# Kernel optimization log

Measured on AMD Instinct MI355X. Metric: run time of the kernel, lower is better.

## Reference

```python
import jax, jax.numpy as jnp
import numpy as np

V = 0.1


def _swap_np():
    d = 2
    s = np.zeros((d * d, d * d))
    for i in range(d):
        for j in range(d):
            s[i * d + j, j * d + i] = 1.0
    k, I = np.kron, np.eye
    s0123 = k(I(d ** 2), s)
    s01234 = k(s0123, I(d))
    s0123456 = k(s01234, s)
    s01234567 = k(s0123456, I(d))
    s0123456789 = k(s01234567, s)
    s012345678911 = k(s0123456789, I(d ** 2))
    s01 = k(s, I(d ** 10))
    s12 = k(k(I(d), s), I(d ** 9))
    s23 = k(k(I(d ** 2), s), I(d ** 8))
    s34 = k(k(I(d ** 3), s), I(d ** 7))
    s45 = k(k(I(d ** 4), s), I(d ** 6))
    s56 = k(k(I(d ** 5), s), I(d ** 5))
    s67 = k(k(I(d ** 6), s), I(d ** 4))
    s78 = k(k(I(d ** 7), s), I(d ** 3))
    s89 = k(k(I(d ** 8), s), I(d ** 2))
    s90 = k(k(I(d ** 9), s), I(d))
    s11 = k(I(d ** 10), s)
    chain = [s01, s12, s23, s34, s45, s56, s67, s78, s89, s90, s11,
             s90, s89, s78, s67, s56, s45, s34, s23, s12, s01]
    swap_far = chain[0]
    for mat in chain[1:]:
        swap_far = swap_far @ mat
    return swap_far @ s012345678911


def _obj_np():
    p = np.zeros((4, 4, 4, 4))
    for q in range(4):
        for w in range(4):
            for e in range(4):
                for r in range(4):
                    if q != w and w != e and e != r and q != r:
                        if q == e or w == r:
                            if q == e and w == r:
                                p[q, w, e, r] = (1 - V) / 2 ** 8
                            else:
                                p[q, w, e, r] = (3 + 5 * V) / (2 ** 8 * 3)
                        else:
                            p[q, w, e, r] = (3 + 13 * V) / (2 ** 8 * 3)
                    else:
                        p[q, w, e, r] = (1 - V) / 2 ** 8
    return p


SWAP = jnp.asarray(_swap_np(), dtype=jnp.float32)   # [4096, 4096] permutation
OBJ = jnp.asarray(_obj_np(), dtype=jnp.float32)     # [4, 4, 4, 4] target distribution
TRIU_R, TRIU_C = np.triu_indices(8, k=1)            # 28 strictly-upper entries, row-major


def setup_inputs() -> dict:
    key = jax.random.key(0)
    # small init keeps POVM element M4 = I - M1 - M2 - M3 near-PSD so the KL log is finite
    params = 0.1 * jax.random.normal(key, (121,), dtype=jnp.float32)
    return {"params": params}


def _generate_state(a):
    a = jnp.exp(a)
    a = a / jnp.linalg.norm(a)                       # F.normalize(dim=0)
    psi = jnp.concatenate([a[0:1], jnp.zeros(3, a.dtype), a[1:5]])  # [8]
    # 4-fold tensor product -> [4096]
    return jnp.kron(jnp.kron(jnp.kron(psi, psi), psi), psi)


def _generate_povm(x):
    eigen = jax.nn.softmax(x[:32].reshape(4, 8), axis=0)  # eigenvalues sum to 1 per column
    offd = x[32:116].reshape(3, 28)

    def make(e, od):
        A = jnp.zeros((8, 8), x.dtype).at[TRIU_R, TRIU_C].set(od)
        A = A - A.T                                  # antisymmetric generator
        U = jax.scipy.linalg.expm(A)                 # orthogonal
        return (U * e[None, :]) @ U.T                # U diag(e) U^T

    m012 = jax.vmap(make)(eigen[:3], offd)           # [3, 8, 8]
    m3 = jnp.eye(8, dtype=x.dtype) - m012.sum(axis=0)
    return jnp.concatenate([m012, m3[None]], axis=0)  # [4, 8, 8]


def reference(params):
    state = _generate_state(params[0:5])             # [4096]
    state = SWAP @ state
    rou = jnp.outer(state, state)                    # [4096, 4096] density matrix
    m = _generate_povm(params[5:121])                # [4, 8, 8]
    # trace(rou @ (Mq (x) Mw (x) Me (x) Mr)) via per-leg contraction instead of
    # 256 dense 4096x4096 matmuls: rou[I,J] * Ma[J,I] with I=(i,j,k,l), J=(m,n,o,p)
    R = rou.reshape((8,) * 8)
    result = jnp.einsum('ijklmnop,qmi,wnj,eok,rpl->qwer', R, m, m, m, m)  # [4,4,4,4]
    y = jnp.sum(OBJ * jnp.log(OBJ / result))         # KL divergence
    return y, result, m
```

## Files before the change

### kernel.cpp

```cpp
#include <hip/hip_runtime.h>
#include <math.h>

#define NT 256


__global__ __launch_bounds__(NT) void qu4_all(const float* __restrict__ P,
                                              float* __restrict__ out)
{
    const int tid  = threadIdx.x;
    const int wave = tid >> 6;
    const int lane = tid & 63;

    __shared__ __align__(16) float XTs[3][96];
    __shared__ __align__(16) float Urow[3][96];
    __shared__ __align__(16) float Esh[32];
    __shared__ __align__(16) float psiF[8];
    __shared__ __align__(16) float Mf[256];
    __shared__ __align__(16) float Tc2[3072];
    __shared__ __align__(16) float Gs[21056];
    __shared__ __align__(16) float Hs[5184];
    __shared__ __align__(16) float HTs[5184];
    __shared__ float redC[16];

    if (wave < 3) {
        const int r = lane >> 3, c = lane & 7;
        float Brow[8];
        #pragma unroll
        for (int u = 0; u < 8; u++) {
            if (u == r)     Brow[u] = 0.f;
            else if (r < u) Brow[u] =  P[37 + wave*28 + (7*r - (r*(r-1))/2 + u - r - 1)];
            else            Brow[u] = -P[37 + wave*28 + (7*u - (u*(u-1))/2 + r - u - 1)];
        }
        float x = ((r == c) ? 1.f : 0.f) + Brow[c] * (1.f / 12.f);
        #pragma unroll
        for (int k = 11; k >= 1; --k) {
            XTs[wave][c*12 + r] = x;
            float4 a0 = *(const float4*)&XTs[wave][c*12];
            float4 a1 = *(const float4*)&XTs[wave][c*12 + 4];
            float d = Brow[0]*a0.x + Brow[1]*a0.y + Brow[2]*a0.z + Brow[3]*a0.w
                    + Brow[4]*a1.x + Brow[5]*a1.y + Brow[6]*a1.z + Brow[7]*a1.w;
            x = ((r == c) ? 1.f : 0.f) + d * (1.f / (float)k);
        }
        Urow[wave][r*12 + c] = x;
    } else {
        if (lane < 8) {
            float x0 = P[5 + lane], x1 = P[13 + lane], x2 = P[21 + lane], x3 = P[29 + lane];
            float mx = fmaxf(fmaxf(x0, x1), fmaxf(x2, x3));
            float e0 = expf(x0-mx), e1 = expf(x1-mx), e2 = expf(x2-mx), e3 = expf(x3-mx);
            float s = e0 + e1 + e2 + e3;
            Esh[lane] = e0/s; Esh[8+lane] = e1/s; Esh[16+lane] = e2/s; Esh[24+lane] = e3/s;
        } else if (lane == 8) {
            float av[5]; float ss = 0.f;
            #pragma unroll
            for (int i = 0; i < 5; i++) { av[i] = expf(P[i]); ss += av[i]*av[i]; }
            float inv = 1.f / sqrtf(ss);
            psiF[0] = av[0]*inv; psiF[1] = 0.f; psiF[2] = 0.f; psiF[3] = 0.f;
            psiF[4] = av[1]*inv; psiF[5] = av[2]*inv; psiF[6] = av[3]*inv; psiF[7] = av[4]*inv;
        }
    }
    __syncthreads();

    {
        const int a = wave, r = lane >> 3, c = lane & 7;
        float m;
        if (a < 3) {
            float4 r0 = *(const float4*)&Urow[a][r*12], r1 = *(const float4*)&Urow[a][r*12+4];
            float4 c0 = *(const float4*)&Urow[a][c*12], c1 = *(const float4*)&Urow[a][c*12+4];
            float4 e0 = *(const float4*)&Esh[a*8],      e1 = *(const float4*)&Esh[a*8+4];
            m = r0.x*e0.x*c0.x + r0.y*e0.y*c0.y + r0.z*e0.z*c0.z + r0.w*e0.w*c0.w
              + r1.x*e1.x*c1.x + r1.y*e1.y*c1.y + r1.z*e1.z*c1.z + r1.w*e1.w*c1.w;
        } else {
            float s = 0.f;
            #pragma unroll
            for (int a2 = 0; a2 < 3; a2++) {
                float4 r0 = *(const float4*)&Urow[a2][r*12], r1 = *(const float4*)&Urow[a2][r*12+4];
                float4 c0 = *(const float4*)&Urow[a2][c*12], c1 = *(const float4*)&Urow[a2][c*12+4];
                float4 e0 = *(const float4*)&Esh[a2*8],      e1 = *(const float4*)&Esh[a2*8+4];
                s += r0.x*e0.x*c0.x + r0.y*e0.y*c0.y + r0.z*e0.z*c0.z + r0.w*e0.w*c0.w
                   + r1.x*e1.x*c1.x + r1.y*e1.y*c1.y + r1.z*e1.z*c1.z + r1.w*e1.w*c1.w;
            }
            m = ((r == c) ? 1.f : 0.f) - s;
        }
        Mf[a*64 + lane] = m;
        out[257 + a*64 + lane] = m;
    }
    __syncthreads();

    {
        const int a = tid >> 6, m = (tid >> 3) & 7, j = tid & 7;
        const int j0 = j >> 2, j1 = (j >> 1) & 1;
        float4 m0 = *(const float4*)&Mf[a*64 + m*8], m1 = *(const float4*)&Mf[a*64 + m*8 + 4];
        float mav[8] = {m0.x,m0.y,m0.z,m0.w, m1.x,m1.y,m1.z,m1.w};
        float4 q0 = *(const float4*)&psiF[0], q1 = *(const float4*)&psiF[4];
        float ps[8] = {q0.x,q0.y,q0.z,q0.w, q1.x,q1.y,q1.z,q1.w};
        float pA[4], pB[4];
        #pragma unroll
        for (int c1 = 0; c1 < 2; c1++)
            #pragma unroll
            for (int i1 = 0; i1 < 2; i1++)
                pA[c1*2+i1] = j0 ? ps[c1*4+i1*2+1] : ps[c1*4+i1*2];
        #pragma unroll
        for (int i2 = 0; i2 < 2; i2++)
            #pragma unroll
            for (int c2 = 0; c2 < 2; c2++)
                pB[i2*2+c2] = j1 ? ps[i2*4+2+c2] : ps[i2*4+c2];
        #pragma unroll
        for (int h = 0; h < 8; h++) {
            const int c1 = h >> 2, c2 = (h >> 1) & 1, r4 = h & 1;
            float v = 0.f;
            #pragma unroll
            for (int i1 = 0; i1 < 2; i1++)
                #pragma unroll
                for (int i2 = 0; i2 < 2; i2++)
                    v += mav[r4*4 + i1*2 + i2] * pA[c1*2+i1] * pB[i2*2+c2];
            Tc2[h*384 + a*96 + m*12 + j] = v;
        }
    }
    __syncthreads();

    if (tid < 128) {
        const int p = tid >> 3, m = tid & 7;
        const int a = p >> 2, b = p & 3;
        float Tv[8][8];
        #pragma unroll
        for (int h = 0; h < 8; h++) {
            float4 t0 = *(const float4*)&Tc2[h*384 + a*96 + m*12];
            float4 t1 = *(const float4*)&Tc2[h*384 + a*96 + m*12 + 4];
            Tv[h][0]=t0.x; Tv[h][1]=t0.y; Tv[h][2]=t0.z; Tv[h][3]=t0.w;
            Tv[h][4]=t1.x; Tv[h][5]=t1.y; Tv[h][6]=t1.z; Tv[h][7]=t1.w;
        }
        float mb[64];
        #pragma unroll
        for (int q = 0; q < 16; q++) {
            float4 v = *(const float4*)&Mf[b*64 + q*4];
            mb[q*4]=v.x; mb[q*4+1]=v.y; mb[q*4+2]=v.z; mb[q*4+3]=v.w;
        }
        #pragma unroll
        for (int n = 0; n < 8; n++) {
            float acc[16];
            #pragma unroll
            for (int t = 0; t < 16; t++) {
                const int h  = (t>>3)*4 + ((t>>2)&1)*2 + (t&1);
                const int r3 = (t>>1)&1;
                acc[t] = mb[n*8 + r3]     * Tv[h][r3]
                       + mb[n*8 + 2 + r3] * Tv[h][2 + r3]
                       + mb[n*8 + 4 + r3] * Tv[h][4 + r3]
                       + mb[n*8 + 6 + r3] * Tv[h][6 + r3];
            }
            float* gp = &Gs[p*1316 + m*164 + n*20];
            *(float4*)&gp[0]  = make_float4(acc[0],  acc[1],  acc[2],  acc[3]);
            *(float4*)&gp[4]  = make_float4(acc[4],  acc[5],  acc[6],  acc[7]);
            *(float4*)&gp[8]  = make_float4(acc[8],  acc[9],  acc[10], acc[11]);
            *(float4*)&gp[12] = make_float4(acc[12], acc[13], acc[14], acc[15]);
        }
    }
    __syncthreads();

    if (tid < 128) {
        const int p = tid >> 3, g = tid & 7;
        const int c1 = g >> 2, c2 = (g >> 1) & 1, r3 = g & 1;
        float4 q0 = *(const float4*)&psiF[0], q1 = *(const float4*)&psiF[4];
        float ps[8] = {q0.x,q0.y,q0.z,q0.w, q1.x,q1.y,q1.z,q1.w};
        float pr[4];
        #pragma unroll
        for (int xx = 0; xx < 4; xx++) pr[xx] = r3 ? ps[4+xx] : ps[xx];
        float acc[2][16];
        #pragma unroll
        for (int t = 0; t < 16; t++) { acc[0][t] = 0.f; acc[1][t] = 0.f; }
        #pragma unroll
        for (int m1 = 0; m1 < 2; m1++)
        #pragma unroll
        for (int m2 = 0; m2 < 2; m2++)
        #pragma unroll
        for (int n0 = 0; n0 < 2; n0++)
        #pragma unroll
        for (int n1 = 0; n1 < 2; n1++) {
            const int m = c2*4 + m1*2 + m2;
            const int n = n0*4 + n1*2 + c1;
            const float* gp = &Gs[p*1316 + m*164 + n*20];
            float4 g0 = *(const float4*)&gp[0],  g1 = *(const float4*)&gp[4];
            float4 g2 = *(const float4*)&gp[8],  g3 = *(const float4*)&gp[12];
            const float w1 = pr[m1*2 + n0];
            const float wa = w1 * ps[m2*4 + n1*2];
            const float wb = w1 * ps[m2*4 + n1*2 + 1];
            float gv[16] = {g0.x,g0.y,g0.z,g0.w, g1.x,g1.y,g1.z,g1.w,
                            g2.x,g2.y,g2.z,g2.w, g3.x,g3.y,g3.z,g3.w};
            #pragma unroll
            for (int t = 0; t < 16; t++) { acc[0][t] += wa*gv[t]; acc[1][t] += wb*gv[t]; }
        }
        #pragma unroll
        for (int r4 = 0; r4 < 2; r4++) {
            const int tV = c1*8 + c2*4 + r3*2 + r4;
            float* hb = &Hs[p*324 + tV*20];
            *(float4*)&hb[0]  = make_float4(acc[r4][0],  acc[r4][1],  acc[r4][2],  acc[r4][3]);
            *(float4*)&hb[4]  = make_float4(acc[r4][4],  acc[r4][5],  acc[r4][6],  acc[r4][7]);
            *(float4*)&hb[8]  = make_float4(acc[r4][8],  acc[r4][9],  acc[r4][10], acc[r4][11]);
            *(float4*)&hb[12] = make_float4(acc[r4][12], acc[r4][13], acc[r4][14], acc[r4][15]);
            #pragma unroll
            for (int t = 0; t < 16; t++) HTs[p*324 + t*20 + tV] = acc[r4][t];
        }
    }
    __syncthreads();

    {
        const int tile = tid >> 4, tv = tid & 15;
        const int tp = tile >> 2, tq = tile & 3;
        float4 hp[4][4];
        #pragma unroll
        for (int i = 0; i < 4; i++) {
            const float* hb = &Hs[(tp*4 + i)*324 + tv*20];
            hp[i][0] = *(const float4*)&hb[0];  hp[i][1] = *(const float4*)&hb[4];
            hp[i][2] = *(const float4*)&hb[8];  hp[i][3] = *(const float4*)&hb[12];
        }
        float acc[4][4];
        #pragma unroll
        for (int jq = 0; jq < 4; jq++) {
            const float* tb = &HTs[(tq*4 + jq)*324 + tv*20];
            float4 h0 = *(const float4*)&tb[0],  h1 = *(const float4*)&tb[4];
            float4 h2 = *(const float4*)&tb[8],  h3 = *(const float4*)&tb[12];
            #pragma unroll
            for (int i = 0; i < 4; i++) {
                acc[i][jq] = hp[i][0].x*h0.x + hp[i][0].y*h0.y + hp[i][0].z*h0.z + hp[i][0].w*h0.w
                           + hp[i][1].x*h1.x + hp[i][1].y*h1.y + hp[i][1].z*h1.z + hp[i][1].w*h1.w
                           + hp[i][2].x*h2.x + hp[i][2].y*h2.y + hp[i][2].z*h2.z + hp[i][2].w*h2.w
                           + hp[i][3].x*h3.x + hp[i][3].y*h3.y + hp[i][3].z*h3.z + hp[i][3].w*h3.w;
            }
        }
        #pragma unroll
        for (int i = 0; i < 4; i++)
            #pragma unroll
            for (int j = 0; j < 4; j++) {
                float v = acc[i][j];
                v += __shfl_xor(v, 1, 64);
                v += __shfl_xor(v, 2, 64);
                v += __shfl_xor(v, 4, 64);
                v += __shfl_xor(v, 8, 64);
                acc[i][j] = v;
            }
        if (tv == 0) {
            float kl = 0.f;
            #pragma unroll
            for (int i = 0; i < 4; i++)
                #pragma unroll
                for (int j = 0; j < 4; j++) {
                    const int idx = (tp*4 + i)*16 + (tq*4 + j);
                    const float Cv = acc[i][j];
                    out[1 + idx] = Cv;
                    const int q = (idx>>6)&3, w = (idx>>4)&3, e = (idx>>2)&3, rr = idx&3;
                    const float OA = 0.9f/256.f, OB = 3.5f/768.f, OC = 4.3f/768.f;
                    float obj;
                    if (q != w && w != e && e != rr && q != rr)
                        obj = (q == e || w == rr) ? ((q == e && w == rr) ? OA : OB) : OC;
                    else obj = OA;
                    kl += obj * logf(obj / Cv);
                }
            redC[tile] = kl;
        }
    }
    __syncthreads();
    if (tid == 0) {
        float s = 0.f;
        #pragma unroll
        for (int i = 0; i < 16; i++) s += redC[i];
        out[0] = s;
    }
}

extern "C" void kernel_launch(void* const* d_in, const int* in_sizes, int n_in,
                              void* d_out, int out_size, void* d_ws, size_t ws_size,
                              hipStream_t stream)
{
    const float* P = (const float*)d_in[0];
    float* out = (float*)d_out;
    qu4_all<<<1, NT, 0, stream>>>(P, out);
}
```

Before: 16.05 us.

## Shorten expm Taylor series, register-only columns, drop barrier, spread stages over 256 threads

The matrix exponential now runs one thread per column. Each thread keeps its own 8x8 generator and column in registers, cutting the Taylor series from 12 terms to 10 and removing the LDS round-trips through XTs. One __syncthreads is removed because each wave computes and consumes its own Mf slice. The G and H contraction stages are split across all 256 threads instead of 128, and the KL log/objective work is spread across 16 lanes with a shuffle reduction. The shorter Taylor series may reduce accuracy for larger generator norms, and the removed barrier depends on each wave reading only the Mf rows it wrote itself.

```diff
diff --git a/kernel.cpp b/kernel.cpp
--- a/kernel.cpp
+++ b/kernel.cpp
@@ -11,8 +11,7 @@
     const int wave = tid >> 6;
     const int lane = tid & 63;
 
-    __shared__ __align__(16) float XTs[3][96];
-    __shared__ __align__(16) float Urow[3][96];
+    __shared__ __align__(16) float Ucol[240];
     __shared__ __align__(16) float Esh[32];
     __shared__ __align__(16) float psiF[8];
     __shared__ __align__(16) float Mf[256];
@@ -22,27 +21,41 @@
     __shared__ __align__(16) float HTs[5184];
     __shared__ float redC[16];
 
-    if (wave < 3) {
-        const int r = lane >> 3, c = lane & 7;
-        float Brow[8];
-        #pragma unroll
-        for (int u = 0; u < 8; u++) {
-            if (u == r)     Brow[u] = 0.f;
-            else if (r < u) Brow[u] =  P[37 + wave*28 + (7*r - (r*(r-1))/2 + u - r - 1)];
-            else            Brow[u] = -P[37 + wave*28 + (7*u - (u*(u-1))/2 + r - u - 1)];
-        }
-        float x = ((r == c) ? 1.f : 0.f) + Brow[c] * (1.f / 12.f);
-        #pragma unroll
-        for (int k = 11; k >= 1; --k) {
-            XTs[wave][c*12 + r] = x;
-            float4 a0 = *(const float4*)&XTs[wave][c*12];
-            float4 a1 = *(const float4*)&XTs[wave][c*12 + 4];
-            float d = Brow[0]*a0.x + Brow[1]*a0.y + Brow[2]*a0.z + Brow[3]*a0.w
-                    + Brow[4]*a1.x + Brow[5]*a1.y + Brow[6]*a1.z + Brow[7]*a1.w;
-            x = ((r == c) ? 1.f : 0.f) + d * (1.f / (float)k);
-        }
-        Urow[wave][r*12 + c] = x;
-    } else {
+    if (wave == 0 && lane < 24) {
+        const int a = lane >> 3, c = lane & 7;
+        const float* Pb = P + 37 + a * 28;
+        float B[8][8];
+        #pragma unroll
+        for (int r = 0; r < 8; r++) {
+            B[r][r] = 0.f;
+            #pragma unroll
+            for (int u = r + 1; u < 8; u++) {
+                float v = Pb[7*r - (r*(r-1))/2 + u - r - 1];
+                B[r][u] = v;  B[u][r] = -v;
+            }
+        }
+        float e[8], col[8];
+        #pragma unroll
+        for (int u = 0; u < 8; u++) { e[u] = (u == c) ? 1.f : 0.f; col[u] = e[u]; }
+        #pragma unroll
+        for (int k = 9; k >= 1; --k) {
+            float nc[8];
+            #pragma unroll
+            for (int r = 0; r < 8; r++) {
+                float s0 = B[r][0]*col[0] + B[r][1]*col[1];
+                float s1 = B[r][2]*col[2] + B[r][3]*col[3];
+                float s2 = B[r][4]*col[4] + B[r][5]*col[5];
+                float s3 = B[r][6]*col[6] + B[r][7]*col[7];
+                nc[r] = (s0 + s1) + (s2 + s3);
+            }
+            const float ik = 1.f / (float)k;
+            #pragma unroll
+            for (int r = 0; r < 8; r++) col[r] = e[r] + nc[r] * ik;
+        }
+        float* uc = &Ucol[a*80 + c*8];
+        *(float4*)&uc[0] = make_float4(col[0], col[1], col[2], col[3]);
+        *(float4*)&uc[4] = make_float4(col[4], col[5], col[6], col[7]);
+    } else if (wave == 1) {
         if (lane < 8) {
             float x0 = P[5 + lane], x1 = P[13 + lane], x2 = P[21 + lane], x3 = P[29 + lane];
             float mx = fmaxf(fmaxf(x0, x1), fmaxf(x2, x3));
@@ -64,30 +77,31 @@
         const int a = wave, r = lane >> 3, c = lane & 7;
         float m;
         if (a < 3) {
-            float4 r0 = *(const float4*)&Urow[a][r*12], r1 = *(const float4*)&Urow[a][r*12+4];
-            float4 c0 = *(const float4*)&Urow[a][c*12], c1 = *(const float4*)&Urow[a][c*12+4];
-            float4 e0 = *(const float4*)&Esh[a*8],      e1 = *(const float4*)&Esh[a*8+4];
-            m = r0.x*e0.x*c0.x + r0.y*e0.y*c0.y + r0.z*e0.z*c0.z + r0.w*e0.w*c0.w
-              + r1.x*e1.x*c1.x + r1.y*e1.y*c1.y + r1.z*e1.z*c1.z + r1.w*e1.w*c1.w;
+            float4 e0 = *(const float4*)&Esh[a*8], e1 = *(const float4*)&Esh[a*8+4];
+            float ev[8] = {e0.x,e0.y,e0.z,e0.w, e1.x,e1.y,e1.z,e1.w};
+            float s = 0.f;
+            #pragma unroll
+            for (int u = 0; u < 8; u++)
+                s += Ucol[a*80 + u*8 + r] * ev[u] * Ucol[a*80 + u*8 + c];
+            m = s;
         } else {
             float s = 0.f;
             #pragma unroll
             for (int a2 = 0; a2 < 3; a2++) {
-                float4 r0 = *(const float4*)&Urow[a2][r*12], r1 = *(const float4*)&Urow[a2][r*12+4];
-                float4 c0 = *(const float4*)&Urow[a2][c*12], c1 = *(const float4*)&Urow[a2][c*12+4];
-                float4 e0 = *(const float4*)&Esh[a2*8],      e1 = *(const float4*)&Esh[a2*8+4];
-                s += r0.x*e0.x*c0.x + r0.y*e0.y*c0.y + r0.z*e0.z*c0.z + r0.w*e0.w*c0.w
-                   + r1.x*e1.x*c1.x + r1.y*e1.y*c1.y + r1.z*e1.z*c1.z + r1.w*e1.w*c1.w;
+                float4 e0 = *(const float4*)&Esh[a2*8], e1 = *(const float4*)&Esh[a2*8+4];
+                float ev[8] = {e0.x,e0.y,e0.z,e0.w, e1.x,e1.y,e1.z,e1.w};
+                #pragma unroll
+                for (int u = 0; u < 8; u++)
+                    s += Ucol[a2*80 + u*8 + r] * ev[u] * Ucol[a2*80 + u*8 + c];
             }
             m = ((r == c) ? 1.f : 0.f) - s;
         }
         Mf[a*64 + lane] = m;
         out[257 + a*64 + lane] = m;
     }
-    __syncthreads();
-
-    {
-        const int a = tid >> 6, m = (tid >> 3) & 7, j = tid & 7;
+
+    {
+        const int a = wave, m = lane >> 3, j = lane & 7;
         const int j0 = j >> 2, j1 = (j >> 1) & 1;
         float4 m0 = *(const float4*)&Mf[a*64 + m*8], m1 = *(const float4*)&Mf[a*64 + m*8 + 4];
         float mav[8] = {m0.x,m0.y,m0.z,m0.w, m1.x,m1.y,m1.z,m1.w};
@@ -118,8 +132,8 @@
     }
     __syncthreads();
 
-    if (tid < 128) {
-        const int p = tid >> 3, m = tid & 7;
+    {
+        const int p = tid >> 4, m = (tid >> 1) & 7, nh = tid & 1;
         const int a = p >> 2, b = p & 3;
         float Tv[8][8];
         #pragma unroll
@@ -129,23 +143,26 @@
             Tv[h][0]=t0.x; Tv[h][1]=t0.y; Tv[h][2]=t0.z; Tv[h][3]=t0.w;
             Tv[h][4]=t1.x; Tv[h][5]=t1.y; Tv[h][6]=t1.z; Tv[h][7]=t1.w;
         }
-        float mb[64];
-        #pragma unroll
-        for (int q = 0; q < 16; q++) {
-            float4 v = *(const float4*)&Mf[b*64 + q*4];
-            mb[q*4]=v.x; mb[q*4+1]=v.y; mb[q*4+2]=v.z; mb[q*4+3]=v.w;
-        }
-        #pragma unroll
-        for (int n = 0; n < 8; n++) {
+        float mb[4][8];
+        #pragma unroll
+        for (int n4 = 0; n4 < 4; n4++) {
+            float4 v0 = *(const float4*)&Mf[b*64 + (nh*4 + n4)*8];
+            float4 v1 = *(const float4*)&Mf[b*64 + (nh*4 + n4)*8 + 4];
+            mb[n4][0]=v0.x; mb[n4][1]=v0.y; mb[n4][2]=v0.z; mb[n4][3]=v0.w;
+            mb[n4][4]=v1.x; mb[n4][5]=v1.y; mb[n4][6]=v1.z; mb[n4][7]=v1.w;
+        }
+        #pragma unroll
+        for (int n4 = 0; n4 < 4; n4++) {
+            const int n = nh*4 + n4;
             float acc[16];
             #pragma unroll
             for (int t = 0; t < 16; t++) {
                 const int h  = (t>>3)*4 + ((t>>2)&1)*2 + (t&1);
                 const int r3 = (t>>1)&1;
-                acc[t] = mb[n*8 + r3]     * Tv[h][r3]
-                       + mb[n*8 + 2 + r3] * Tv[h][2 + r3]
-                       + mb[n*8 + 4 + r3] * Tv[h][4 + r3]
-                       + mb[n*8 + 6 + r3] * Tv[h][6 + r3];
+                acc[t] = mb[n4][r3]   * Tv[h][r3]
+                       + mb[n4][2+r3] * Tv[h][2+r3]
+                       + mb[n4][4+r3] * Tv[h][4+r3]
+                       + mb[n4][6+r3] * Tv[h][6+r3];
             }
             float* gp = &Gs[p*1316 + m*164 + n*20];
             *(float4*)&gp[0]  = make_float4(acc[0],  acc[1],  acc[2],  acc[3]);
@@ -156,17 +173,17 @@
     }
     __syncthreads();
 
-    if (tid < 128) {
-        const int p = tid >> 3, g = tid & 7;
+    {
+        const int p = tid >> 4, g = (tid >> 1) & 7, hh = tid & 1;
         const int c1 = g >> 2, c2 = (g >> 1) & 1, r3 = g & 1;
         float4 q0 = *(const float4*)&psiF[0], q1 = *(const float4*)&psiF[4];
         float ps[8] = {q0.x,q0.y,q0.z,q0.w, q1.x,q1.y,q1.z,q1.w};
         float pr[4];
         #pragma unroll
         for (int xx = 0; xx < 4; xx++) pr[xx] = r3 ? ps[4+xx] : ps[xx];
-        float acc[2][16];
-        #pragma unroll
-        for (int t = 0; t < 16; t++) { acc[0][t] = 0.f; acc[1][t] = 0.f; }
+        float acc0[8], acc1[8];
+        #pragma unroll
+        for (int t = 0; t < 8; t++) { acc0[t] = 0.f; acc1[t] = 0.f; }
         #pragma unroll
         for (int m1 = 0; m1 < 2; m1++)
         #pragma unroll
@@ -177,27 +194,28 @@
         for (int n1 = 0; n1 < 2; n1++) {
             const int m = c2*4 + m1*2 + m2;
             const int n = n0*4 + n1*2 + c1;
-            const float* gp = &Gs[p*1316 + m*164 + n*20];
-            float4 g0 = *(const float4*)&gp[0],  g1 = *(const float4*)&gp[4];
-            float4 g2 = *(const float4*)&gp[8],  g3 = *(const float4*)&gp[12];
+            const float* gp = &Gs[p*1316 + m*164 + n*20 + hh*8];
+            float4 g0 = *(const float4*)&gp[0], g1 = *(const float4*)&gp[4];
             const float w1 = pr[m1*2 + n0];
             const float wa = w1 * ps[m2*4 + n1*2];
             const float wb = w1 * ps[m2*4 + n1*2 + 1];
-            float gv[16] = {g0.x,g0.y,g0.z,g0.w, g1.x,g1.y,g1.z,g1.w,
-                            g2.x,g2.y,g2.z,g2.w, g3.x,g3.y,g3.z,g3.w};
-            #pragma unroll
-            for (int t = 0; t < 16; t++) { acc[0][t] += wa*gv[t]; acc[1][t] += wb*gv[t]; }
-        }
-        #pragma unroll
-        for (int r4 = 0; r4 < 2; r4++) {
-            const int tV = c1*8 + c2*4 + r3*2 + r4;
-            float* hb = &Hs[p*324 + tV*20];
-            *(float4*)&hb[0]  = make_float4(acc[r4][0],  acc[r4][1],  acc[r4][2],  acc[r4][3]);
-            *(float4*)&hb[4]  = make_float4(acc[r4][4],  acc[r4][5],  acc[r4][6],  acc[r4][7]);
-            *(float4*)&hb[8]  = make_float4(acc[r4][8],  acc[r4][9],  acc[r4][10], acc[r4][11]);
-            *(float4*)&hb[12] = make_float4(acc[r4][12], acc[r4][13], acc[r4][14], acc[r4][15]);
-            #pragma unroll
-            for (int t = 0; t < 16; t++) HTs[p*324 + t*20 + tV] = acc[r4][t];
+            float gv[8] = {g0.x,g0.y,g0.z,g0.w, g1.x,g1.y,g1.z,g1.w};
+            #pragma unroll
+            for (int t = 0; t < 8; t++) { acc0[t] += wa*gv[t]; acc1[t] += wb*gv[t]; }
+        }
+        {
+            const int tV0 = c1*8 + c2*4 + r3*2;
+            float* hb0 = &Hs[p*324 + tV0*20 + hh*8];
+            *(float4*)&hb0[0] = make_float4(acc0[0], acc0[1], acc0[2], acc0[3]);
+            *(float4*)&hb0[4] = make_float4(acc0[4], acc0[5], acc0[6], acc0[7]);
+            float* hb1 = &Hs[p*324 + (tV0+1)*20 + hh*8];
+            *(float4*)&hb1[0] = make_float4(acc1[0], acc1[1], acc1[2], acc1[3]);
+            *(float4*)&hb1[4] = make_float4(acc1[4], acc1[5], acc1[6], acc1[7]);
+            #pragma unroll
+            for (int t = 0; t < 8; t++) {
+                HTs[p*324 + (hh*8 + t)*20 + tV0]     = acc0[t];
+                HTs[p*324 + (hh*8 + t)*20 + tV0 + 1] = acc1[t];
+            }
         }
     }
     __syncthreads();
@@ -237,25 +255,27 @@
                 v += __shfl_xor(v, 8, 64);
                 acc[i][j] = v;
             }
-        if (tv == 0) {
-            float kl = 0.f;
-            #pragma unroll
-            for (int i = 0; i < 4; i++)
-                #pragma unroll
-                for (int j = 0; j < 4; j++) {
-                    const int idx = (tp*4 + i)*16 + (tq*4 + j);
-                    const float Cv = acc[i][j];
-                    out[1 + idx] = Cv;
-                    const int q = (idx>>6)&3, w = (idx>>4)&3, e = (idx>>2)&3, rr = idx&3;
-                    const float OA = 0.9f/256.f, OB = 3.5f/768.f, OC = 4.3f/768.f;
-                    float obj;
-                    if (q != w && w != e && e != rr && q != rr)
-                        obj = (q == e || w == rr) ? ((q == e && w == rr) ? OA : OB) : OC;
-                    else obj = OA;
-                    kl += obj * logf(obj / Cv);
-                }
-            redC[tile] = kl;
-        }
+        const int li = tv >> 2, lj = tv & 3;
+        float Cv = 0.f;
+        #pragma unroll
+        for (int i = 0; i < 4; i++)
+            #pragma unroll
+            for (int j = 0; j < 4; j++)
+                if (li == i && lj == j) Cv = acc[i][j];
+        const int idx = (tp*4 + li)*16 + (tq*4 + lj);
+        out[1 + idx] = Cv;
+        const int q = (idx>>6)&3, w = (idx>>4)&3, e = (idx>>2)&3, rr = idx&3;
+        const float OA = 0.9f/256.f, OB = 3.5f/768.f, OC = 4.3f/768.f;
+        float obj;
+        if (q != w && w != e && e != rr && q != rr)
+            obj = (q == e || w == rr) ? ((q == e && w == rr) ? OA : OB) : OC;
+        else obj = OA;
+        float klt = obj * logf(obj / Cv);
+        klt += __shfl_xor(klt, 1, 64);
+        klt += __shfl_xor(klt, 2, 64);
+        klt += __shfl_xor(klt, 4, 64);
+        klt += __shfl_xor(klt, 8, 64);
+        if (tv == 0) redC[tile] = klt;
     }
     __syncthreads();
     if (tid == 0) {
```

Measured after the change: 13.38 us. 1.2x faster.
